# Kernel tuning notes

Measured on AMD Instinct MI355X. Metric: run time of the kernel, lower is better.

Reference implementation:

```python
import jax, jax.numpy as jnp
import numpy as np

EPS = 1e-5

def _conv1x1(x, w, b):
    # x: (B,C,H,W), w: (O,C), b: (O,)
    return jnp.einsum('bchw,oc->bohw', x, w) + b[None, :, None, None]

def _maxpool2(x):
    B, C, H, W = x.shape
    return x.reshape(B, C, H // 2, 2, W // 2, 2).max(axis=(3, 5))

def setup_inputs() -> dict:
    key = jax.random.key(0)
    ks = jax.random.split(key, 12)
    B, C, Ci, H, W = 8, 256, 128, 64, 64
    s = lambda k, shape, scale: jax.random.normal(k, shape, jnp.float32) * scale
    return {
        'x': s(ks[0], (B, C, H, W), 1.0),
        'neighborFeat': s(ks[1], (B, C, H, W), 1.0),
        'g_w': s(ks[2], (Ci, C), 0.05), 'g_b': jnp.zeros((Ci,), jnp.float32),
        'theta_w': s(ks[3], (Ci, C), 0.05), 'theta_b': jnp.zeros((Ci,), jnp.float32),
        'phi_w': s(ks[4], (Ci, C), 0.05), 'phi_b': jnp.zeros((Ci,), jnp.float32),
        'w_w': s(ks[5], (C, Ci), 0.05), 'w_b': jnp.zeros((C,), jnp.float32),
        'bn_gamma': s(ks[6], (C,), 0.1) + 1.0,
        'bn_beta': s(ks[7], (C,), 0.1),
        'bn_mean': s(ks[8], (C,), 0.1),
        'bn_var': jax.random.uniform(ks[9], (C,), jnp.float32, 0.5, 1.5),
    }

def reference(x, neighborFeat, g_w, g_b, theta_w, theta_b, phi_w, phi_b,
              w_w, w_b, bn_gamma, bn_beta, bn_mean, bn_var):
    B, C, H, W = x.shape
    Ci = g_w.shape[0]
    # g: conv1x1 on x then maxpool2 -> (B, Nkv, Ci)
    g_x = _maxpool2(_conv1x1(x, g_w, g_b)).reshape(B, Ci, -1).transpose(0, 2, 1)
    # theta: conv1x1 on neighborFeat, full res -> (B, Nq, Ci)
    theta_x = _conv1x1(neighborFeat, theta_w, theta_b).reshape(B, Ci, -1).transpose(0, 2, 1)
    # phi: conv1x1 on neighborFeat then maxpool2 -> (B, Ci, Nkv)
    phi_x = _maxpool2(_conv1x1(neighborFeat, phi_w, phi_b)).reshape(B, Ci, -1)
    f = jnp.einsum('bqc,bck->bqk', theta_x, phi_x)       # (B, Nq, Nkv)
    f_div_C = jax.nn.softmax(f, axis=-1)
    y = jnp.einsum('bqk,bkc->bqc', f_div_C, g_x)          # (B, Nq, Ci)
    y = y.transpose(0, 2, 1).reshape(B, Ci, H, W)
    # W: conv1x1 + BatchNorm (eval mode with running stats)
    wy = _conv1x1(y, w_w, w_b)
    wy = (wy - bn_mean[None, :, None, None]) * (bn_gamma[None, :, None, None]
          * jax.lax.rsqrt(bn_var + EPS)[None, :, None, None]) + bn_beta[None, :, None, None]
    return wy + x
```

## Files before the change

kernel.cpp:

```cpp
#include <hip/hip_runtime.h>

typedef __attribute__((ext_vector_type(8))) short short8;
typedef __attribute__((ext_vector_type(4))) short short4v;
typedef __attribute__((ext_vector_type(4))) float f32x4;
typedef __attribute__((ext_vector_type(16))) float f32x16;
typedef __attribute__((ext_vector_type(4))) unsigned u32x4;

__device__ __forceinline__ float bf2f(short s) {
  union { unsigned u; float f; } cv;
  cv.u = ((unsigned)(unsigned short)s) << 16;
  return cv.f;
}
__device__ __forceinline__ short f2bf(float f) {
  union { float f; unsigned u; } cv;
  cv.f = f;
  unsigned r = (cv.u + 0x7fffu + ((cv.u >> 16) & 1u)) >> 16;
  return (short)(unsigned short)r;
}
__device__ __forceinline__ unsigned pk2(float a, float b) {
  return (unsigned)(unsigned short)f2bf(a) | ((unsigned)(unsigned short)f2bf(b) << 16);
}

#define MFMA16(a, b, c) __builtin_amdgcn_mfma_f32_16x16x32_bf16((a), (b), (c), 0, 0, 0)
#define MFMA32(a, b, c) __builtin_amdgcn_mfma_f32_32x32x16_bf16((a), (b), (c), 0, 0, 0)

__global__ __launch_bounds__(256) void cvt_w(
    const float* __restrict__ s0, const float* __restrict__ s1,
    const float* __restrict__ s2, const float* __restrict__ s3,
    short* __restrict__ d)
{
  const float* srcs[4] = {s0, s1, s2, s3};
  const float* s = srcs[blockIdx.y];
  int i = (blockIdx.x * 256 + threadIdx.x) * 4;
  f32x4 v = *reinterpret_cast<const f32x4*>(s + i);
  short4v o;
  #pragma unroll
  for (int j = 0; j < 4; j++) o[j] = f2bf(v[j]);
  *reinterpret_cast<short4v*>(d + (size_t)blockIdx.y * 32768 + i) = o;
}

template <int NPROJ, int MODE1>
__device__ __forceinline__ void conv_body(
    short (*in_t)[40], short (*wt)[40],
    const float* __restrict__ in,
    const short* __restrict__ w0, const float* __restrict__ bias0,
    const short* __restrict__ w1, const float* __restrict__ bias1,
    short* __restrict__ out0, short* __restrict__ out1)
{
  const int b = blockIdx.y;
  const int p0 = blockIdx.x * 128;
  const int tid = threadIdx.x;
  const int wave = tid >> 6, lane = tid & 63;
  const int lr = lane & 15, lg = lane >> 4;

  const short* wsrc[2] = {w0, w1};

  f32x4 acc[NPROJ][8];
  #pragma unroll
  for (int pj = 0; pj < NPROJ; pj++)
    #pragma unroll
    for (int n = 0; n < 8; n++) acc[pj][n] = (f32x4)0.0f;

  for (int kc = 0; kc < 256; kc += 32) {
    __syncthreads();
    {
      int c = tid >> 4;
      int pg = (tid & 15) * 8;
      const float* src = in + ((size_t)(b * 256 + kc + c)) * 4096 + p0 + pg;
      f32x4 v0 = *reinterpret_cast<const f32x4*>(src);
      f32x4 v1 = *reinterpret_cast<const f32x4*>(src + 4);
      #pragma unroll
      for (int j = 0; j < 8; j++) {
        int p = pg + j;
        int a = ((p & 63) >> 1) * 4 + ((p >> 6) << 1) + (p & 1);
        float fv = (j < 4) ? v0[j] : v1[j - 4];
        in_t[a][c ^ ((((a >> 3) & 3)) << 3)] = f2bf(fv);
      }
    }
    if (tid < NPROJ * 128) {
      int pj = tid >> 7, o = tid & 127;
      const short8* src = reinterpret_cast<const short8*>(wsrc[pj] + (size_t)o * 256 + kc);
      int f = (o >> 3) & 3;
      #pragma unroll
      for (int gq = 0; gq < 4; gq++)
        *reinterpret_cast<short8*>(&wt[pj * 128 + o][(gq ^ f) * 8]) = src[gq];
    }
    __syncthreads();

    int arow = wave * 16 + lr;
    short8 afrag = *reinterpret_cast<const short8*>(
        &in_t[arow][(lg ^ ((arow >> 3) & 3)) * 8]);
    #pragma unroll
    for (int pj = 0; pj < NPROJ; pj++) {
      #pragma unroll
      for (int n = 0; n < 8; n++) {
        int brow = n * 16 + lr;
        short8 bfrag = *reinterpret_cast<const short8*>(
            &wt[pj * 128 + brow][(lg ^ ((brow >> 3) & 3)) * 8]);
        acc[pj][n] = MFMA16(afrag, bfrag, acc[pj][n]);
      }
    }
  }

  const float* bsrc[2] = {bias0, bias1};
  short* osrc[2] = {out0, out1};
  const int kp = blockIdx.x * 32 + wave * 4 + lg;
  #pragma unroll
  for (int pj = 0; pj < NPROJ; pj++) {
    const int mode = (pj == 0 && NPROJ == 2) ? 0 : MODE1;
    #pragma unroll
    for (int n = 0; n < 8; n++) {
      int o = n * 16 + lr;
      float bv = bsrc[pj][o];
      if (mode == 0) {
        #pragma unroll
        for (int r = 0; r < 4; r++) {
          int pix = (wave * 4 + lg) * 2 + (r & 1) + ((r >> 1) & 1) * 64;
          osrc[pj][((size_t)b * 4096 + p0 + pix) * 128 + o] = f2bf(acc[pj][n][r] + bv);
        }
      } else {
        f32x4 v = acc[pj][n];
        float pv = fmaxf(fmaxf(v[0], v[1]), fmaxf(v[2], v[3])) + bv;
        if (mode == 1)
          osrc[pj][((size_t)b * 1024 + kp) * 128 + o] = f2bf(pv);
        else
          osrc[pj][((size_t)b * 128 + o) * 1024 + kp] = f2bf(pv);
      }
    }
  }
}

__global__ __launch_bounds__(512, 4) void conv_all(
    const float* __restrict__ nb, const float* __restrict__ x,
    const short* __restrict__ th_w, const float* __restrict__ th_b,
    const short* __restrict__ ph_w, const float* __restrict__ ph_b,
    const short* __restrict__ g_w, const float* __restrict__ g_b,
    short* __restrict__ theta, short* __restrict__ phi_kc,
    short* __restrict__ g_ck)
{
  __shared__ short in_t[128][40];
  __shared__ short wt[256][40];
  if (blockIdx.z == 0)
    conv_body<2, 1>(in_t, wt, nb, th_w, th_b, ph_w, ph_b, theta, phi_kc);
  else
    conv_body<1, 2>(in_t, wt, x, g_w, g_b, nullptr, nullptr, g_ck, nullptr);
}

__global__ __launch_bounds__(512) void attn(
    const short* __restrict__ theta, const short* __restrict__ phi,
    const short* __restrict__ g, short* __restrict__ y)
{
  __shared__ char lds[131072];
  __shared__ float ml[8][32][2];

  const int b = blockIdx.y;
  const int q0 = blockIdx.x * 128;
  const int tid = threadIdx.x;
  const int wave = tid >> 6, lane = tid & 63;
  const int l31 = lane & 31, hi = lane >> 5;
  const int zw = wave >> 2, wq = wave & 3;

  short8 ath[8];
  {
    const short* tq = theta + ((size_t)b * 4096 + q0 + wq * 32 + l31) * 128 + hi * 8;
    #pragma unroll
    for (int s = 0; s < 8; s++)
      ath[s] = *reinterpret_cast<const short8*>(tq + s * 16);
  }

  const int t8 = tid & 255, zs = tid >> 8;
  const int pr = t8 >> 2, pcq = t8 & 3;
  const int gr = t8 >> 1, ghq = t8 & 1;
  const short* phi_src = phi + ((size_t)b * 1024 + zs * 512 + pr) * 128 + pcq * 32;
  const short* g_src   = g + ((size_t)b * 128 + gr) * 1024 + zs * 512 + ghq * 32;

  short8 sphi[4], sg[4];
  #pragma unroll
  for (int j = 0; j < 4; j++) {
    sphi[j] = *reinterpret_cast<const short8*>(phi_src + j * 8);
    sg[j]   = *reinterpret_cast<const short8*>(g_src + j * 8);
  }

  float mrun = -1e30f, lpart = 0.0f;
  f32x16 acc[4];
  #pragma unroll
  for (int n = 0; n < 4; n++) acc[n] = (f32x16)0.0f;

  {
    char* pb = lds + zs * 16384;
    char* gb = lds + 65536 + zs * 16384;
    #pragma unroll
    for (int j = 0; j < 4; j++) {
      *reinterpret_cast<short8*>(pb + pr * 256 + (((pcq * 4 + j) ^ (pr & 15)) * 16)) = sphi[j];
      *reinterpret_cast<short8*>(gb + gr * 128 + (((ghq * 4 + j) ^ (gr & 7)) * 16)) = sg[j];
    }
  }

  for (int t = 0; t < 8; t++) {
    __syncthreads();
    char* pb = lds + ((t & 1) * 2 + zw) * 16384;
    char* gb = lds + 65536 + ((t & 1) * 2 + zw) * 16384;

    if (t < 7) {
      const short* ps = phi_src + (t + 1) * 64 * 128;
      const short* gs = g_src + (t + 1) * 64;
      #pragma unroll
      for (int j = 0; j < 4; j++) {
        sphi[j] = *reinterpret_cast<const short8*>(ps + j * 8);
        sg[j]   = *reinterpret_cast<const short8*>(gs + j * 8);
      }
    }

    f32x16 facc0 = (f32x16)0.0f, facc1 = (f32x16)0.0f;
    __builtin_amdgcn_s_setprio(1);
    #pragma unroll
    for (int s = 0; s < 8; s++) {
      int slot = (s << 1) | hi;
      short8 pf0 = *reinterpret_cast<const short8*>(
          pb + l31 * 256 + ((slot ^ (l31 & 15)) * 16));
      short8 pf1 = *reinterpret_cast<const short8*>(
          pb + (32 + l31) * 256 + ((slot ^ (l31 & 15)) * 16));
      facc0 = MFMA32(pf0, ath[s], facc0);
      facc1 = MFMA32(pf1, ath[s], facc1);
    }
    __builtin_amdgcn_s_setprio(0);

    float m = facc0[0];
    #pragma unroll
    for (int r = 1; r < 16; r++) m = fmaxf(m, facc0[r]);
    #pragma unroll
    for (int r = 0; r < 16; r++) m = fmaxf(m, facc1[r]);
    m = fmaxf(m, __shfl_xor(m, 32));
    if (__any(m - mrun > 10.0f)) {
      float mn = fmaxf(mrun, m);
      float sc = __expf(mrun - mn);
      mrun = mn;
      lpart *= sc;
      #pragma unroll
      for (int reg = 0; reg < 16; reg++) {
        int qr = (reg & 3) + 8 * (reg >> 2) + 4 * hi;
        float sr = __shfl(sc, qr);
        #pragma unroll
        for (int n = 0; n < 4; n++) acc[n][reg] *= sr;
      }
    }
    float ls = 0.0f;
    #pragma unroll
    for (int r = 0; r < 16; r++) { facc0[r] = __expf(facc0[r] - mrun); ls += facc0[r]; }
    #pragma unroll
    for (int r = 0; r < 16; r++) { facc1[r] = __expf(facc1[r] - mrun); ls += facc1[r]; }
    lpart += ls;

    __builtin_amdgcn_s_setprio(1);
    #pragma unroll
    for (int s = 0; s < 4; s++) {
      const int base = (s & 1) * 8;
      float p0, p1, p2, p3, p4, p5, p6, p7;
      if (s < 2) {
        p0 = facc0[base + 0]; p1 = facc0[base + 1]; p2 = facc0[base + 2]; p3 = facc0[base + 3];
        p4 = facc0[base + 4]; p5 = facc0[base + 5]; p6 = facc0[base + 6]; p7 = facc0[base + 7];
      } else {
        p0 = facc1[base + 0]; p1 = facc1[base + 1]; p2 = facc1[base + 2]; p3 = facc1[base + 3];
        p4 = facc1[base + 4]; p5 = facc1[base + 5]; p6 = facc1[base + 6]; p7 = facc1[base + 7];
      }
      unsigned P0w0 = pk2(p0, p1), P0w1 = pk2(p2, p3);
      unsigned P1w0 = pk2(p4, p5), P1w1 = pk2(p6, p7);
      unsigned x0 = (unsigned)__shfl_xor((int)P0w0, 32);
      unsigned x1 = (unsigned)__shfl_xor((int)P0w1, 32);
      unsigned y0 = (unsigned)__shfl_xor((int)P1w0, 32);
      unsigned y1 = (unsigned)__shfl_xor((int)P1w1, 32);
      union { u32x4 u; short8 s8; } pf;
      pf.u[0] = hi ? y0 : P0w0;
      pf.u[1] = hi ? y1 : P0w1;
      pf.u[2] = hi ? P1w0 : x0;
      pf.u[3] = hi ? P1w1 : x1;
      int slot = (s << 1) | hi;
      #pragma unroll
      for (int n = 0; n < 4; n++) {
        int rg = n * 32 + l31;
        short8 gf = *reinterpret_cast<const short8*>(
            gb + rg * 128 + ((slot ^ (rg & 7)) * 16));
        acc[n] = MFMA32(pf.s8, gf, acc[n]);
      }
    }
    __builtin_amdgcn_s_setprio(0);

    if (t < 7) {
      char* pb2 = lds + (((t + 1) & 1) * 2 + zs) * 16384;
      char* gb2 = lds + 65536 + (((t + 1) & 1) * 2 + zs) * 16384;
      #pragma unroll
      for (int j = 0; j < 4; j++) {
        *reinterpret_cast<short8*>(pb2 + pr * 256 + (((pcq * 4 + j) ^ (pr & 15)) * 16)) = sphi[j];
        *reinterpret_cast<short8*>(gb2 + gr * 128 + (((ghq * 4 + j) ^ (gr & 7)) * 16)) = sg[j];
      }
    }
  }

  float lsum = lpart + __shfl_xor(lpart, 32);
  if (lane < 32) { ml[wave][l31][0] = mrun; ml[wave][l31][1] = lsum; }
  __syncthreads();
  float mo = ml[wave ^ 4][l31][0];
  float lo = ml[wave ^ 4][l31][1];
  float M = fmaxf(mrun, mo);
  float e0 = __expf(mrun - M), e1 = __expf(mo - M);
  float wown = e0 / (e0 * lsum + e1 * lo);
  #pragma unroll
  for (int reg = 0; reg < 16; reg++) {
    int qr = (reg & 3) + 8 * (reg >> 2) + 4 * hi;
    float wr = __shfl(wown, qr);
    #pragma unroll
    for (int n = 0; n < 4; n++) acc[n][reg] *= wr;
  }
  float* mb = (float*)(lds + wq * 16384);
  if (zw == 1) {
    #pragma unroll
    for (int n = 0; n < 4; n++)
      #pragma unroll
      for (int reg = 0; reg < 16; reg++) {
        int qrow = (reg & 3) + 8 * (reg >> 2) + 4 * hi;
        mb[qrow * 128 + n * 32 + l31] = acc[n][reg];
      }
  }
  __syncthreads();
  if (zw == 0) {
    #pragma unroll
    for (int n = 0; n < 4; n++)
      #pragma unroll
      for (int reg = 0; reg < 16; reg++) {
        int qrow = (reg & 3) + 8 * (reg >> 2) + 4 * hi;
        float v = acc[n][reg] + mb[qrow * 128 + n * 32 + l31];
        y[((size_t)b * 4096 + q0 + wq * 32 + qrow) * 128 + n * 32 + l31] = f2bf(v);
      }
  }
}

__global__ __launch_bounds__(512) void wconv_bn(
    const short* __restrict__ yb, const short* __restrict__ ww,
    const float* __restrict__ wb,
    const float* __restrict__ gamma, const float* __restrict__ beta,
    const float* __restrict__ mean, const float* __restrict__ var,
    const float* __restrict__ x, float* __restrict__ out)
{
  __shared__ short y_s[128][136];
  __shared__ float sc_s[256];
  __shared__ float sh_s[256];

  const int b = blockIdx.y;
  const int q0 = blockIdx.x * 128;
  const int tid = threadIdx.x;
  const int wave = tid >> 6, lane = tid & 63;
  const int lr = lane & 15, lg = lane >> 4;

  {
    int r = tid >> 2, c0 = (tid & 3) * 32;
    const short8* src = reinterpret_cast<const short8*>(
        yb + ((size_t)(b * 4096 + q0 + r)) * 128 + c0);
    short8* dst = reinterpret_cast<short8*>(&y_s[r][c0]);
    #pragma unroll
    for (int j = 0; j < 4; j++) dst[j] = src[j];
    if (tid < 256) {
      float s = gamma[tid] * rsqrtf(var[tid] + 1e-5f);
      sc_s[tid] = s;
      sh_s[tid] = (wb[tid] - mean[tid]) * s + beta[tid];
    }
  }
  __syncthreads();

  f32x4 acc[2][8];
  #pragma unroll
  for (int m = 0; m < 2; m++)
    #pragma unroll
    for (int n = 0; n < 8; n++) acc[m][n] = (f32x4)0.0f;

  #pragma unroll
  for (int kk = 0; kk < 4; kk++) {
    short8 af[2], bfr[8];
    #pragma unroll
    for (int m = 0; m < 2; m++)
      af[m] = *reinterpret_cast<const short8*>(
          ww + (size_t)(wave * 32 + m * 16 + lr) * 128 + kk * 32 + lg * 8);
    #pragma unroll
    for (int n = 0; n < 8; n++)
      bfr[n] = *reinterpret_cast<const short8*>(&y_s[n * 16 + lr][kk * 32 + lg * 8]);
    #pragma unroll
    for (int m = 0; m < 2; m++)
      #pragma unroll
      for (int n = 0; n < 8; n++)
        acc[m][n] = MFMA16(af[m], bfr[n], acc[m][n]);
  }

  #pragma unroll
  for (int m = 0; m < 2; m++) {
    #pragma unroll
    for (int n = 0; n < 8; n++) {
      #pragma unroll
      for (int r = 0; r < 4; r++) {
        int co = wave * 32 + m * 16 + lg * 4 + r;
        int q = q0 + n * 16 + lr;
        size_t oidx = ((size_t)b * 256 + co) * 4096 + q;
        float v = acc[m][n][r] * sc_s[co] + sh_s[co];
        out[oidx] = v + x[oidx];
      }
    }
  }
}

extern "C" void kernel_launch(void* const* d_in, const int* in_sizes, int n_in,
                              void* d_out, int out_size, void* d_ws, size_t ws_size,
                              hipStream_t stream)
{
  const float* x    = (const float*)d_in[0];
  const float* nb   = (const float*)d_in[1];
  const float* g_w  = (const float*)d_in[2];
  const float* g_b  = (const float*)d_in[3];
  const float* th_w = (const float*)d_in[4];
  const float* th_b = (const float*)d_in[5];
  const float* ph_w = (const float*)d_in[6];
  const float* ph_b = (const float*)d_in[7];
  const float* w_w  = (const float*)d_in[8];
  const float* w_b  = (const float*)d_in[9];
  const float* gam  = (const float*)d_in[10];
  const float* bet  = (const float*)d_in[11];
  const float* mu   = (const float*)d_in[12];
  const float* var  = (const float*)d_in[13];
  float* out = (float*)d_out;

  char* ws = (char*)d_ws;
  short* theta_full = (short*)(ws);
  short* yb         = (short*)(ws + (size_t)(8u << 20));
  short* phi_kc     = (short*)(ws + (size_t)(16u << 20));
  short* g_ck       = (short*)(ws + (size_t)(18u << 20));
  short* wts        = (short*)(ws + (size_t)(20u << 20));
  short* th_wb = wts;
  short* ph_wb = wts + 32768;
  short* g_wb  = wts + 2 * 32768;
  short* w_wb  = wts + 3 * 32768;

  cvt_w<<<dim3(32, 4), 256, 0, stream>>>(th_w, ph_w, g_w, w_w, wts);
  conv_all<<<dim3(32, 8, 2), 512, 0, stream>>>(nb, x, th_wb, th_b, ph_wb, ph_b,
                                               g_wb, g_b, theta_full, phi_kc, g_ck);
  attn<<<dim3(32, 8), 512, 0, stream>>>(theta_full, phi_kc, g_ck, yb);
  wconv_bn<<<dim3(32, 8), 512, 0, stream>>>(yb, w_wb, w_b, gam, bet, mu, var, x, out);
}
```

Measured before the change: 82.44 us.

## Stream phi/g tiles straight into LDS, use hardware bf16 pack, and tree-reduce softmax

The attention kernel now copies phi and g tiles from global memory directly into LDS with global_load_lds, using pre-swizzled source addresses. This replaces the register staging and the later ds_write stores. The per-tile max and sum reductions become pairwise trees to shorten dependency chains, and the bf16 packing uses v_cvt_pk_bf16_f32 in place of a software rounding path. Direct-to-LDS loads free registers and VALU work, but their completion depends on the existing barrier and vmcnt behaviour. Nothing else in the code guarantees that completion.

```diff
diff --git a/kernel.cpp b/kernel.cpp
--- a/kernel.cpp
+++ b/kernel.cpp
@@ -17,8 +17,15 @@
   unsigned r = (cv.u + 0x7fffu + ((cv.u >> 16) & 1u)) >> 16;
   return (short)(unsigned short)r;
 }
-__device__ __forceinline__ unsigned pk2(float a, float b) {
-  return (unsigned)(unsigned short)f2bf(a) | ((unsigned)(unsigned short)f2bf(b) << 16);
+__device__ __forceinline__ unsigned cvtpk(float a, float b) {
+  unsigned r;
+  asm("v_cvt_pk_bf16_f32 %0, %1, %2" : "=v"(r) : "v"(a), "v"(b));
+  return r;
+}
+__device__ __forceinline__ void load_lds16(const void* g, void* l) {
+  __builtin_amdgcn_global_load_lds(
+      (const __attribute__((address_space(1))) void*)g,
+      (__attribute__((address_space(3))) void*)l, 16, 0, 0);
 }
 
 #define MFMA16(a, b, c) __builtin_amdgcn_mfma_f32_16x16x32_bf16((a), (b), (c), 0, 0, 0)
@@ -168,17 +175,23 @@
       ath[s] = *reinterpret_cast<const short8*>(tq + s * 16);
   }
 
-  const int t8 = tid & 255, zs = tid >> 8;
-  const int pr = t8 >> 2, pcq = t8 & 3;
-  const int gr = t8 >> 1, ghq = t8 & 1;
-  const short* phi_src = phi + ((size_t)b * 1024 + zs * 512 + pr) * 128 + pcq * 32;
-  const short* g_src   = g + ((size_t)b * 128 + gr) * 1024 + zs * 512 + ghq * 32;
-
-  short8 sphi[4], sg[4];
-  #pragma unroll
-  for (int j = 0; j < 4; j++) {
-    sphi[j] = *reinterpret_cast<const short8*>(phi_src + j * 8);
-    sg[j]   = *reinterpret_cast<const short8*>(g_src + j * 8);
+  const short* psrc[4];
+  {
+    int rb = wq * 16 + (lane >> 4), sl = lane & 15;
+    #pragma unroll
+    for (int i = 0; i < 4; i++) {
+      int r = rb + i * 4;
+      psrc[i] = phi + ((size_t)b * 1024 + zw * 512 + r) * 128 + ((sl ^ (r & 15)) * 8);
+    }
+  }
+  const short* gsrc[4];
+  {
+    int rb = wq * 32 + (lane >> 3), sl = lane & 7;
+    #pragma unroll
+    for (int i = 0; i < 4; i++) {
+      int r = rb + i * 8;
+      gsrc[i] = g + ((size_t)b * 128 + r) * 1024 + zw * 512 + ((sl ^ (r & 7)) * 8);
+    }
   }
 
   float mrun = -1e30f, lpart = 0.0f;
@@ -187,12 +200,12 @@
   for (int n = 0; n < 4; n++) acc[n] = (f32x16)0.0f;
 
   {
-    char* pb = lds + zs * 16384;
-    char* gb = lds + 65536 + zs * 16384;
-    #pragma unroll
-    for (int j = 0; j < 4; j++) {
-      *reinterpret_cast<short8*>(pb + pr * 256 + (((pcq * 4 + j) ^ (pr & 15)) * 16)) = sphi[j];
-      *reinterpret_cast<short8*>(gb + gr * 128 + (((ghq * 4 + j) ^ (gr & 7)) * 16)) = sg[j];
+    char* pb = lds + zw * 16384 + wq * 4096;
+    char* gb = lds + 65536 + zw * 16384 + wq * 4096;
+    #pragma unroll
+    for (int i = 0; i < 4; i++) {
+      load_lds16(psrc[i], pb + i * 1024);
+      load_lds16(gsrc[i], gb + i * 1024);
     }
   }
 
@@ -202,12 +215,12 @@
     char* gb = lds + 65536 + ((t & 1) * 2 + zw) * 16384;
 
     if (t < 7) {
-      const short* ps = phi_src + (t + 1) * 64 * 128;
-      const short* gs = g_src + (t + 1) * 64;
-      #pragma unroll
-      for (int j = 0; j < 4; j++) {
-        sphi[j] = *reinterpret_cast<const short8*>(ps + j * 8);
-        sg[j]   = *reinterpret_cast<const short8*>(gs + j * 8);
+      char* pb2 = lds + (((t + 1) & 1) * 2 + zw) * 16384 + wq * 4096;
+      char* gb2 = lds + 65536 + (((t + 1) & 1) * 2 + zw) * 16384 + wq * 4096;
+      #pragma unroll
+      for (int i = 0; i < 4; i++) {
+        load_lds16(psrc[i] + (t + 1) * 8192, pb2 + i * 1024);
+        load_lds16(gsrc[i] + (t + 1) * 64, gb2 + i * 1024);
       }
     }
 
@@ -225,12 +238,15 @@
     }
     __builtin_amdgcn_s_setprio(0);
 
-    float m = facc0[0];
-    #pragma unroll
-    for (int r = 1; r < 16; r++) m = fmaxf(m, facc0[r]);
-    #pragma unroll
-    for (int r = 0; r < 16; r++) m = fmaxf(m, facc1[r]);
-    m = fmaxf(m, __shfl_xor(m, 32));
+    float mv[16];
+    #pragma unroll
+    for (int r = 0; r < 16; r++) mv[r] = fmaxf(facc0[r], facc1[r]);
+    #pragma unroll
+    for (int s = 8; s >= 1; s >>= 1)
+      #pragma unroll
+      for (int r = 0; r < s; r++) mv[r] = fmaxf(mv[r], mv[r + s]);
+    float m = fmaxf(mv[0], __shfl_xor(mv[0], 32));
+
     if (__any(m - mrun > 10.0f)) {
       float mn = fmaxf(mrun, m);
       float sc = __expf(mrun - mn);
@@ -244,12 +260,20 @@
         for (int n = 0; n < 4; n++) acc[n][reg] *= sr;
       }
     }
-    float ls = 0.0f;
-    #pragma unroll
-    for (int r = 0; r < 16; r++) { facc0[r] = __expf(facc0[r] - mrun); ls += facc0[r]; }
-    #pragma unroll
-    for (int r = 0; r < 16; r++) { facc1[r] = __expf(facc1[r] - mrun); ls += facc1[r]; }
-    lpart += ls;
+    #pragma unroll
+    for (int r = 0; r < 16; r++) facc0[r] = __expf(facc0[r] - mrun);
+    #pragma unroll
+    for (int r = 0; r < 16; r++) facc1[r] = __expf(facc1[r] - mrun);
+    {
+      float sv[16];
+      #pragma unroll
+      for (int r = 0; r < 16; r++) sv[r] = facc0[r] + facc1[r];
+      #pragma unroll
+      for (int s = 8; s >= 1; s >>= 1)
+        #pragma unroll
+        for (int r = 0; r < s; r++) sv[r] += sv[r + s];
+      lpart += sv[0];
+    }
 
     __builtin_amdgcn_s_setprio(1);
     #pragma unroll
@@ -263,8 +287,8 @@
         p0 = facc1[base + 0]; p1 = facc1[base + 1]; p2 = facc1[base + 2]; p3 = facc1[base + 3];
         p4 = facc1[base + 4]; p5 = facc1[base + 5]; p6 = facc1[base + 6]; p7 = facc1[base + 7];
       }
-      unsigned P0w0 = pk2(p0, p1), P0w1 = pk2(p2, p3);
-      unsigned P1w0 = pk2(p4, p5), P1w1 = pk2(p6, p7);
+      unsigned P0w0 = cvtpk(p0, p1), P0w1 = cvtpk(p2, p3);
+      unsigned P1w0 = cvtpk(p4, p5), P1w1 = cvtpk(p6, p7);
       unsigned x0 = (unsigned)__shfl_xor((int)P0w0, 32);
       unsigned x1 = (unsigned)__shfl_xor((int)P0w1, 32);
       unsigned y0 = (unsigned)__shfl_xor((int)P1w0, 32);
@@ -284,16 +308,6 @@
       }
     }
     __builtin_amdgcn_s_setprio(0);
-
-    if (t < 7) {
-      char* pb2 = lds + (((t + 1) & 1) * 2 + zs) * 16384;
-      char* gb2 = lds + 65536 + (((t + 1) & 1) * 2 + zs) * 16384;
-      #pragma unroll
-      for (int j = 0; j < 4; j++) {
-        *reinterpret_cast<short8*>(pb2 + pr * 256 + (((pcq * 4 + j) ^ (pr & 15)) * 16)) = sphi[j];
-        *reinterpret_cast<short8*>(gb2 + gr * 128 + (((ghq * 4 + j) ^ (gr & 7)) * 16)) = sg[j];
-      }
-    }
   }
 
   float lsum = lpart + __shfl_xor(lpart, 32);
```

Measured after the change: 82.38 us. About the same (-0.1%).
